# Kernel tuning notes

Measured on AMD Instinct MI355X. Metric: run time of the kernel, lower is better.

Reference implementation:

```python
import jax, jax.numpy as jnp
import numpy as np

EPS = 0.01  # diffusion sampling noise scale


def gru_last(x, Wx, Wh, bx, bh):
    """Run a single-layer GRU (torch gate conventions) over x: [B, L, C] -> final hidden [B, H]."""
    B, L, C = x.shape
    H = Wh.shape[0]
    xg = jnp.einsum('blc,cg->blg', x, Wx) + bx  # precomputed input gates [B, L, 3H]

    def step(h, xg_t):
        hg = h @ Wh + bh
        xr, xz, xn = jnp.split(xg_t, 3, axis=-1)
        hr, hz, hn = jnp.split(hg, 3, axis=-1)
        r = jax.nn.sigmoid(xr + hr)
        z = jax.nn.sigmoid(xz + hz)
        n = jnp.tanh(xn + r * hn)
        h_new = (1.0 - z) * n + z * h
        return h_new, None

    h0 = jnp.zeros((B, H), x.dtype)
    h, _ = jax.lax.scan(step, h0, jnp.swapaxes(xg, 0, 1))
    return h


def gru_aggr(x, Wx, Wh, bx, bh, Wo, bo):
    return gru_last(x, Wx, Wh, bx, bh) @ Wo + bo


def setup_inputs() -> dict:
    key = jax.random.key(0)
    N, C, DEG, H, C_OUT, T = 8000, 64, 16, 128, 64, 4
    ks = jax.random.split(key, 16)

    def lin(k, fan_in, shape):
        return jax.random.normal(k, shape, dtype=jnp.float32) / np.sqrt(fan_in)

    inp = {
        'node_attr': jax.random.normal(ks[0], (N, C), dtype=jnp.float32),
        'neighbors': jax.random.randint(ks[1], (N, DEG), 0, N, dtype=jnp.int32),
        'noise': jax.random.normal(ks[2], (T, N, DEG), dtype=jnp.float32),
        # diff_aggr GRU + output head (edge log-prob comes from channel 0)
        'dWx': lin(ks[3], C, (C, 3 * H)),
        'dWh': lin(ks[4], H, (H, 3 * H)),
        'dbx': jnp.zeros((3 * H,), jnp.float32),
        'dbh': jnp.zeros((3 * H,), jnp.float32),
        'dWo': lin(ks[5], H, (H, C_OUT)),
        'dbo': jnp.zeros((C_OUT,), jnp.float32),
        # walk_aggr GRU + output head (node embedding)
        'wWx': lin(ks[6], C, (C, 3 * H)),
        'wWh': lin(ks[7], H, (H, 3 * H)),
        'wbx': jnp.zeros((3 * H,), jnp.float32),
        'wbh': jnp.zeros((3 * H,), jnp.float32),
        'wWo': lin(ks[8], H, (H, C_OUT)),
        'wbo': jnp.zeros((C_OUT,), jnp.float32),
    }
    return inp


def reference(node_attr, neighbors, noise,
              dWx, dWh, dbx, dbh, dWo, dbo,
              wWx, wWh, wbx, wbh, wWo, wbo):
    N, C = node_attr.shape
    DEG = neighbors.shape[1]
    T = noise.shape[0]

    cur = jnp.arange(N)                      # current frontier of each walk
    walk_embeds = node_attr[:, None, :]      # [N, L, C], L grows each step
    logps = []
    for t in range(T):
        nbr = neighbors[cur]                 # [N, DEG] candidate next hops
        cand = node_attr[nbr]                # [N, DEG, C]
        L = walk_embeds.shape[1]
        prefix = jnp.broadcast_to(walk_embeds[:, None], (N, DEG, L, C))
        seq = jnp.concatenate([prefix, cand[:, :, None, :]], axis=2)  # [N, DEG, L+1, C]
        seq = seq.reshape(N * DEG, L + 1, C)
        logp = gru_aggr(seq, dWx, dWh, dbx, dbh, dWo, dbo)[:, 0].reshape(N, DEG)
        # per-source-node log-softmax normalizer (no_grad in original)
        norm = jax.lax.stop_gradient(jax.nn.logsumexp(logp, axis=1, keepdims=True))
        logp = logp - norm
        p = jnp.exp(logp)
        noisy = p + EPS * noise[t]
        sel = jnp.argmax(noisy, axis=1)      # scatter_max over each node's candidates
        logps.append(jnp.take_along_axis(logp, sel[:, None], axis=1)[:, 0])
        cur = jnp.take_along_axis(nbr, sel[:, None], axis=1)[:, 0]
        walk_embeds = jnp.concatenate([walk_embeds, node_attr[cur][:, None, :]], axis=1)

    walks_logp = jnp.stack(logps, axis=1)    # [N, T]
    v_out = gru_aggr(walk_embeds, wWx, wWh, wbx, wbh, wWo, wbo)  # [N, C_OUT]
    return v_out, walks_logp
```

## Files before the change

### kernel.cpp

```cpp
#include <hip/hip_runtime.h>
#include <math.h>

#define NN 8000
#define CD 64
#define DG 16
#define HD 128
#define G3 384
#define TT 4
#define MARGIN 4e-3f

#if __has_builtin(__builtin_amdgcn_rcpf)
#define RCP(x) __builtin_amdgcn_rcpf(x)
#else
#define RCP(x) (1.f/(x))
#endif

__device__ __forceinline__ float fsig (float x){ return RCP(1.f + __expf(-x)); }
__device__ __forceinline__ float ftanh(float x){ return 1.f - 2.f*RCP(1.f + __expf(2.f*x)); }

__device__ __forceinline__ double fexp64(double x){
    const double LOG2E  = 1.4426950408889634074;
    const double LN2_HI = 6.93147180369123816490e-01;
    const double LN2_LO = 1.90821492927058770002e-10;
    x = fmin(fmax(x, -700.0), 700.0);
    double fn = rint(x * LOG2E);
    double r  = fma(-fn, LN2_HI, x);
    r = fma(-fn, LN2_LO, r);
    double p = 1.6059043836821613e-10;
    p = fma(p, r, 2.0876756987868099e-09);
    p = fma(p, r, 2.5052108385441719e-08);
    p = fma(p, r, 2.7557319223985893e-07);
    p = fma(p, r, 2.7557319223985888e-06);
    p = fma(p, r, 2.4801587301587302e-05);
    p = fma(p, r, 1.9841269841269841e-04);
    p = fma(p, r, 1.3888888888888889e-03);
    p = fma(p, r, 8.3333333333333332e-03);
    p = fma(p, r, 4.1666666666666664e-02);
    p = fma(p, r, 1.6666666666666666e-01);
    p = fma(p, r, 0.5);
    p = fma(p, r, 1.0);
    p = fma(p, r, 1.0);
    long long bits = __double_as_longlong(p) + ((long long)(int)fn << 52);
    return __longlong_as_double(bits);
}
__device__ __forceinline__ double sig64f (double x){ return 1.0/(1.0 + fexp64(-x)); }
__device__ __forceinline__ double tanh64f(double x){ return 1.0 - 2.0/(fexp64(2.0*x) + 1.0); }

__global__ __launch_bounds__(384) void xg_kernel(const float* __restrict__ A,
    const float* __restrict__ W, const float* __restrict__ b,
    float* __restrict__ hiP, float* __restrict__ loP)
{
    __shared__ float a_s[8][64];
    const int g  = threadIdx.x;
    const int l  = g & 63, q = g >> 6;
    const int n0 = blockIdx.x * 8;
    for (int idx = threadIdx.x; idx < 8*64; idx += 384)
        a_s[idx>>6][idx&63] = A[(size_t)n0*64 + idx];
    __syncthreads();
    double acc[8];
    const double bg = (double)b[g];
#pragma unroll
    for (int j=0;j<8;j++) acc[j] = bg;
    for (int c=0;c<64;c++){
        const double w = (double)W[c*G3 + g];
#pragma unroll
        for (int j=0;j<8;j++) acc[j] += (double)a_s[j][c]*w;
    }
#pragma unroll
    for (int j=0;j<8;j++){
        const size_t base = (size_t)(n0+j)*64 + l;
        const float hi = (float)acc[j];
        hiP[base*8 + q] = hi;
        if (q < 2) hiP[base*8 + 6 + q] = 0.f;
        if (loP) loP[base*6 + q] = (float)(acc[j] - (double)hi);
    }
}

__global__ __launch_bounds__(256) void repack_kernel(const float* __restrict__ W,
                                                     float* __restrict__ P)
{
    const int idx = blockIdx.x*256 + threadIdx.x;
    const int k = idx >> 9, rem = idx & 511, l = rem >> 3, s = rem & 7;
    P[idx] = (s < 6) ? W[k*G3 + s*64 + l] : 0.f;
}

__global__ __launch_bounds__(256) void walk_kernel(
    const int*   __restrict__ nbrs,  const float* __restrict__ noise,
    const float* __restrict__ XGfP,  const float* __restrict__ dWhP,
    const float* __restrict__ dbh,   const float* __restrict__ dWo,
    const float* __restrict__ dbo,
    int* __restrict__ paths, int* __restrict__ fail_cnt, int* __restrict__ fail_list,
    float* __restrict__ out)
{
    __shared__ float hf_s[4][HD];
    __shared__ float part_s[4][4][6][64];

    const int wid  = threadIdx.x >> 6;
    const int lane = threadIdx.x & 63;
    const int node = blockIdx.x*4 + wid;

    float h0 = 0.f, h1 = 0.f;
    float dbhf[6], hgf[6];
#pragma unroll
    for (int m=0;m<6;m++){ dbhf[m] = dbh[lane+64*m]; hgf[m] = dbhf[m]; }
    const float wo0f0 = dWo[lane*CD];
    const float wo0f1 = dWo[(lane+64)*CD];
    const float dbo0f = dbo[0];

    int  cur = node;
    int  ch0=0, ch1=0, ch2=0, ch3=0;
    bool pushed = false;

    for (int t=0;t<TT;t++){
        if      (t==0) ch0 = cur;
        else if (t==1) ch1 = cur;
        else if (t==2) ch2 = cur;
        else           ch3 = cur;

        {
            const float4* xr = (const float4*)(XGfP + ((size_t)cur*64 + lane)*8);
            const float4 A = xr[0], B = xr[1];
            float r = fsig (A.x + hgf[0]);
            float z = fsig (A.z + hgf[2]);
            float n = ftanh(B.x + r*hgf[4]);
            h0 = (1.f-z)*n + z*h0;
            r = fsig (A.y + hgf[1]);
            z = fsig (A.w + hgf[3]);
            n = ftanh(B.y + r*hgf[5]);
            h1 = (1.f-z)*n + z*h1;
        }
        hf_s[wid][lane] = h0;  hf_s[wid][lane+64] = h1;
        __syncthreads();

        {
            float pacc[4][6];
#pragma unroll
            for (int j=0;j<4;j++)
#pragma unroll
                for (int m=0;m<6;m++) pacc[j][m] = 0.f;
            const float4* wr = (const float4*)(dWhP + (size_t)lane*8);
#pragma unroll 4
            for (int kk=0; kk<32; kk++){
                const int k = wid*32 + kk;
                const float4 W0 = wr[k*128], W1 = wr[k*128+1];
#pragma unroll
                for (int j=0;j<4;j++){
                    const float hk = hf_s[j][k];
                    pacc[j][0] += hk*W0.x; pacc[j][1] += hk*W0.y;
                    pacc[j][2] += hk*W0.z; pacc[j][3] += hk*W0.w;
                    pacc[j][4] += hk*W1.x; pacc[j][5] += hk*W1.y;
                }
            }
#pragma unroll
            for (int j=0;j<4;j++)
#pragma unroll
                for (int m=0;m<6;m++) part_s[wid][j][m][lane] = pacc[j][m];
        }
        __syncthreads();

#pragma unroll
        for (int m=0;m<6;m++)
            hgf[m] = dbhf[m] + part_s[0][wid][m][lane] + part_s[1][wid][m][lane]
                             + part_s[2][wid][m][lane] + part_s[3][wid][m][lane];

        int   nbrv = (lane < DG) ? nbrs[(size_t)cur*DG + lane] : 0;
        float nz   = (lane < DG) ? noise[((size_t)t*NN + node)*DG + lane] : 0.f;
        float lf = -3.0e38f;
#pragma unroll
        for (int g=0; g<4; g++){
            float4 CA[4], CB[4];
#pragma unroll
            for (int j=0;j<4;j++){
                const int nd = __shfl(nbrv, g*4+j);
                const float4* cr = (const float4*)(XGfP + ((size_t)nd*64 + lane)*8);
                CA[j] = cr[0];  CB[j] = cr[1];
            }
            float part[4];
#pragma unroll
            for (int j=0;j<4;j++){
                float r = fsig (CA[j].x + hgf[0]);
                float z = fsig (CA[j].z + hgf[2]);
                float n = ftanh(CB[j].x + r*hgf[4]);
                part[j]  = ((1.f-z)*n + z*h0) * wo0f0;
                r = fsig (CA[j].y + hgf[1]);
                z = fsig (CA[j].w + hgf[3]);
                n = ftanh(CB[j].y + r*hgf[5]);
                part[j] += ((1.f-z)*n + z*h1) * wo0f1;
            }
#pragma unroll
            for (int off=32; off>0; off>>=1){
#pragma unroll
                for (int j=0;j<4;j++) part[j] += __shfl_xor(part[j], off);
            }
#pragma unroll
            for (int j=0;j<4;j++) if (lane == g*4+j) lf = part[j] + dbo0f;
        }

        float v  = (lane < DG) ? lf : -3.0e38f;
        float mx = v;
#pragma unroll
        for (int off=32; off>0; off>>=1) mx = fmaxf(mx, __shfl_xor(mx, off));
        float e = (lane < DG) ? __expf(v - mx) : 0.f;
        float s = e;
#pragma unroll
        for (int off=32; off>0; off>>=1) s += __shfl_xor(s, off);
        const float normf = mx + __logf(s);

        float noisyf = (lane < DG) ? __expf(v - normf) + 0.01f*nz : -3.0e38f;
        int   idx = lane;
        float bv  = noisyf;
#pragma unroll
        for (int off=32; off>0; off>>=1){
            float ov = __shfl_xor(bv, off);
            int   oi = __shfl_xor(idx, off);
            if (ov > bv || (ov == bv && oi < idx)){ bv = ov; idx = oi; }
        }
        float sv = (lane == idx || lane >= DG) ? -3.0e38f : noisyf;
#pragma unroll
        for (int off=32; off>0; off>>=1) sv = fmaxf(sv, __shfl_xor(sv, off));

        const bool trip = (bv - sv) < MARGIN;
        if (trip && !pushed){
            if (lane == 0){
                const int slot = atomicAdd(fail_cnt, 1);
                if (slot < NN) fail_list[slot] = node | (t << 16);
            }
            pushed = true;
        }

        const float lpf = __shfl(v, idx) - normf;
        if (lane == 0) out[NN*CD + node*TT + t] = lpf;
        cur = __shfl(nbrv, idx);
    }

    if (lane == 0){
        int* p = paths + (size_t)node*8;
        p[0]=ch0; p[1]=ch1; p[2]=ch2; p[3]=ch3; p[4]=cur;
    }
}

__global__ __launch_bounds__(256) void fix_kernel(
    const int*   __restrict__ nbrs,  const float* __restrict__ noise,
    const float* __restrict__ XGfP,  const float* __restrict__ XGrP,
    const float* __restrict__ dWhP,  const float* __restrict__ dbh,
    const float* __restrict__ dWo,   const float* __restrict__ dbo,
    const int* __restrict__ fail_cnt, const int* __restrict__ fail_list,
    int* __restrict__ paths, float* __restrict__ out)
{
    __shared__ double h_s[4][HD];
    __shared__ double part_s[4][4][6][64];

    const int wid  = threadIdx.x >> 6;
    const int lane = threadIdx.x & 63;
    const int count = min(fail_cnt[0], NN);
    if (blockIdx.x*4 >= count) return;

    const int  ii     = blockIdx.x*4 + wid;
    const bool active = (ii < count);
    const int  entry  = active ? fail_list[ii] : fail_list[0];
    const int  node   = entry & 0xFFFF;
    const int  t0     = active ? (entry >> 16) : TT;
    const int* pw     = paths + (size_t)node*8;

    double db64[6];
#pragma unroll
    for (int m=0;m<6;m++) db64[m] = (double)dbh[lane+64*m];
    const double wo0d0 = (double)dWo[lane*CD];
    const double wo0d1 = (double)dWo[(lane+64)*CD];
    const double dbo0d = (double)dbo[0];

    double H0 = 0.0, H1 = 0.0;
    double g64[6];
#pragma unroll
    for (int m=0;m<6;m++) g64[m] = db64[m];
    int cur = node;
    int c0=0,c1=0,c2=0,c3=0;

    for (int t=0;t<TT;t++){
        if      (t==0) c0 = cur;
        else if (t==1) c1 = cur;
        else if (t==2) c2 = cur;
        else           c3 = cur;

        {
            const size_t base = (size_t)cur*64 + lane;
            const float* hi = XGfP + base*8;
            const float* lo = XGrP + base*6;
            double r = sig64f (((double)hi[0]+(double)lo[0]) + g64[0]);
            double z = sig64f (((double)hi[2]+(double)lo[2]) + g64[2]);
            double n = tanh64f(((double)hi[4]+(double)lo[4]) + r*g64[4]);
            H0 = (1.0-z)*n + z*H0;
            r = sig64f (((double)hi[1]+(double)lo[1]) + g64[1]);
            z = sig64f (((double)hi[3]+(double)lo[3]) + g64[3]);
            n = tanh64f(((double)hi[5]+(double)lo[5]) + r*g64[5]);
            H1 = (1.0-z)*n + z*H1;
        }
        h_s[wid][lane] = H0;  h_s[wid][lane+64] = H1;
        __syncthreads();

        {
            double pacc[4][6];
#pragma unroll
            for (int j=0;j<4;j++)
#pragma unroll
                for (int m=0;m<6;m++) pacc[j][m] = 0.0;
            const float4* wr = (const float4*)(dWhP + (size_t)lane*8);
#pragma unroll 4
            for (int kk=0; kk<32; kk++){
                const int k = wid*32 + kk;
                const float4 W0 = wr[k*128], W1 = wr[k*128+1];
#pragma unroll
                for (int j=0;j<4;j++){
                    const double hk = h_s[j][k];
                    pacc[j][0] += hk*(double)W0.x; pacc[j][1] += hk*(double)W0.y;
                    pacc[j][2] += hk*(double)W0.z; pacc[j][3] += hk*(double)W0.w;
                    pacc[j][4] += hk*(double)W1.x; pacc[j][5] += hk*(double)W1.y;
                }
            }
#pragma unroll
            for (int j=0;j<4;j++)
#pragma unroll
                for (int m=0;m<6;m++) part_s[wid][j][m][lane] = pacc[j][m];
        }
        __syncthreads();

#pragma unroll
        for (int m=0;m<6;m++)
            g64[m] = db64[m] + part_s[0][wid][m][lane] + part_s[1][wid][m][lane]
                             + part_s[2][wid][m][lane] + part_s[3][wid][m][lane];

        if (t < t0){
            cur = pw[t+1];
            continue;
        }

        int   nbrv = (lane < DG) ? nbrs[(size_t)cur*DG + lane] : 0;
        float nz   = (lane < DG) ? noise[((size_t)t*NN + node)*DG + lane] : 0.f;
        double lv = -1e300;
#pragma unroll
        for (int g=0; g<4; g++){
            float ch[4][6], cl[4][6];
#pragma unroll
            for (int j=0;j<4;j++){
                const int nd = __shfl(nbrv, g*4+j);
                const size_t base = (size_t)nd*64 + lane;
                const float* hi = XGfP + base*8;
                const float* lo = XGrP + base*6;
#pragma unroll
                for (int q=0;q<6;q++){ ch[j][q]=hi[q]; cl[j][q]=lo[q]; }
            }
#pragma unroll
            for (int j=0;j<4;j++){
                double r = sig64f (((double)ch[j][0]+(double)cl[j][0]) + g64[0]);
                double z = sig64f (((double)ch[j][2]+(double)cl[j][2]) + g64[2]);
                double n = tanh64f(((double)ch[j][4]+(double)cl[j][4]) + r*g64[4]);
                double part = ((1.0-z)*n + z*H0) * wo0d0;
                r = sig64f (((double)ch[j][1]+(double)cl[j][1]) + g64[1]);
                z = sig64f (((double)ch[j][3]+(double)cl[j][3]) + g64[3]);
                n = tanh64f(((double)ch[j][5]+(double)cl[j][5]) + r*g64[5]);
                part += ((1.0-z)*n + z*H1) * wo0d1;
#pragma unroll
                for (int off=32; off>0; off>>=1) part += __shfl_xor(part, off);
                if (lane == g*4+j) lv = part + dbo0d;
            }
        }

        double dv = (lane < DG) ? lv : -1e300;
        double dmx = dv;
#pragma unroll
        for (int off=32; off>0; off>>=1) dmx = fmax(dmx, __shfl_xor(dmx, off));
        double de = (lane < DG) ? fexp64(dv - dmx) : 0.0;
        double ds = de;
#pragma unroll
        for (int off=32; off>0; off>>=1) ds += __shfl_xor(ds, off);
        const double dnorm = dmx + log(ds);
        double dnoisy = (lane < DG) ? fexp64(dv - dnorm) + 0.01*(double)nz : -1e300;
        int di = lane;
#pragma unroll
        for (int off=32; off>0; off>>=1){
            double ov = __shfl_xor(dnoisy, off);
            int    oi = __shfl_xor(di, off);
            if (ov > dnoisy || (ov == dnoisy && oi < di)){ dnoisy = ov; di = oi; }
        }
        const double lpfix = __shfl(dv, di) - dnorm;
        if (active && lane == 0) out[NN*CD + node*TT + t] = (float)lpfix;
        cur = __shfl(nbrv, di);
    }

    if (active && lane == 0){
        int* p = paths + (size_t)node*8;
        p[0]=c0; p[1]=c1; p[2]=c2; p[3]=c3; p[4]=cur;
    }
}

__global__ __launch_bounds__(256) void wgru_kernel(
    const int*   __restrict__ paths, const float* __restrict__ XGwP,
    const float* __restrict__ wWhP,  const float* __restrict__ wbh,
    const float* __restrict__ wWo,   const float* __restrict__ wbo,
    float* __restrict__ out)
{
    __shared__ float hw_s[4][HD];
    __shared__ float part_s[4][4][6][64];
    const int wid  = threadIdx.x >> 6;
    const int lane = threadIdx.x & 63;
    const int node = blockIdx.x*4 + wid;

    float h0 = 0.f, h1 = 0.f;
    float wb[6], hg[6];
#pragma unroll
    for (int m=0;m<6;m++){ wb[m] = wbh[lane+64*m]; hg[m] = wb[m]; }
    const int* p = paths + (size_t)node*8;

#pragma unroll
    for (int s=0; s<=TT; s++){
        const int c = p[s];
        const float4* xr = (const float4*)(XGwP + ((size_t)c*64 + lane)*8);
        const float4 A = xr[0], B = xr[1];
        float r = fsig (A.x + hg[0]);
        float z = fsig (A.z + hg[2]);
        float n = ftanh(B.x + r*hg[4]);
        h0 = (1.f-z)*n + z*h0;
        r = fsig (A.y + hg[1]);
        z = fsig (A.w + hg[3]);
        n = ftanh(B.y + r*hg[5]);
        h1 = (1.f-z)*n + z*h1;
        if (s < TT){
            hw_s[wid][lane] = h0;  hw_s[wid][lane+64] = h1;
            __syncthreads();
            float pacc[4][6];
#pragma unroll
            for (int j=0;j<4;j++)
#pragma unroll
                for (int m=0;m<6;m++) pacc[j][m] = 0.f;
            const float4* wr = (const float4*)(wWhP + (size_t)lane*8);
#pragma unroll 4
            for (int kk=0; kk<32; kk++){
                const int k = wid*32 + kk;
                const float4 W0 = wr[k*128], W1 = wr[k*128+1];
#pragma unroll
                for (int j=0;j<4;j++){
                    const float hk = hw_s[j][k];
                    pacc[j][0] += hk*W0.x; pacc[j][1] += hk*W0.y;
                    pacc[j][2] += hk*W0.z; pacc[j][3] += hk*W0.w;
                    pacc[j][4] += hk*W1.x; pacc[j][5] += hk*W1.y;
                }
            }
#pragma unroll
            for (int j=0;j<4;j++)
#pragma unroll
                for (int m=0;m<6;m++) part_s[wid][j][m][lane] = pacc[j][m];
            __syncthreads();
#pragma unroll
            for (int m=0;m<6;m++)
                hg[m] = wb[m] + part_s[0][wid][m][lane] + part_s[1][wid][m][lane]
                              + part_s[2][wid][m][lane] + part_s[3][wid][m][lane];
        }
    }
    hw_s[wid][lane] = h0;  hw_s[wid][lane+64] = h1;
    __syncthreads();

    float acc = wbo[lane];
    const float* wcol = wWo + lane;
    for (int i=0;i<HD;i++) acc += hw_s[wid][i] * wcol[(size_t)i*CD];
    out[(size_t)node*CD + lane] = acc;
}

extern "C" void kernel_launch(void* const* d_in, const int* in_sizes, int n_in,
                              void* d_out, int out_size, void* d_ws, size_t ws_size,
                              hipStream_t stream)
{
    const float* attr  = (const float*)d_in[0];
    const int*   nbrs  = (const int*)  d_in[1];
    const float* noise = (const float*)d_in[2];
    const float* dWx = (const float*)d_in[3];
    const float* dWh = (const float*)d_in[4];
    const float* dbx = (const float*)d_in[5];
    const float* dbh = (const float*)d_in[6];
    const float* dWo = (const float*)d_in[7];
    const float* dbo = (const float*)d_in[8];
    const float* wWx = (const float*)d_in[9];
    const float* wWh = (const float*)d_in[10];
    const float* wbx = (const float*)d_in[11];
    const float* wbh = (const float*)d_in[12];
    const float* wWo = (const float*)d_in[13];
    const float* wbo = (const float*)d_in[14];
    float* out = (float*)d_out;

    char* ws = (char*)d_ws;
    float* XGfP      = (float*)(ws);
    float* XGrP      = (float*)(ws + 16384000);
    float* XGwP      = (float*)(ws + 28672000);
    float* dWhP      = (float*)(ws + 45056000);
    float* wWhP      = (float*)(ws + 45318144);
    int*   paths     = (int*)  (ws + 45580288);
    int*   fail_list = (int*)  (ws + 45836288);
    int*   fail_cnt  = (int*)  (ws + 45868288);

    hipMemsetAsync(fail_cnt, 0, sizeof(int), stream);

    xg_kernel<<<NN/8, G3, 0, stream>>>(attr, dWx, dbx, XGfP, XGrP);
    xg_kernel<<<NN/8, G3, 0, stream>>>(attr, wWx, wbx, XGwP, nullptr);
    repack_kernel<<<(HD*64*8)/256, 256, 0, stream>>>(dWh, dWhP);
    repack_kernel<<<(HD*64*8)/256, 256, 0, stream>>>(wWh, wWhP);

    walk_kernel<<<NN/4, 256, 0, stream>>>(nbrs, noise, XGfP, dWhP,
                                          dbh, dWo, dbo,
                                          paths, fail_cnt, fail_list, out);
    fix_kernel<<<2000, 256, 0, stream>>>(nbrs, noise, XGfP, XGrP,
                                         dWhP, dbh, dWo, dbo,
                                         fail_cnt, fail_list, paths, out);
    wgru_kernel<<<NN/4, 256, 0, stream>>>(paths, XGwP, wWhP, wbh, wWo, wbo, out);
}
```

Before: 529.1 us.

## Fuse fix-up and walk GRU into one tail kernel with per-node trip flags

Merges the fp64 fix-up pass and the walk-embedding GRU into a single launch. Non-tripped nodes run the walk GRU in their own blocks, while a fixed pool of blocks grid-strides over the failure list and runs the walk GRU right after recomputing each path. This removes one launch and serialization point, so fix-up work overlaps with the bulk walk GRU. The fp64 partial-sum reduction is also reshaped into two stages to cut shared memory, which adds extra syncs. In exchange, fix-up blocks now loop serially, so a long failure list could lengthen the tail.

```diff
diff --git a/kernel.cpp b/kernel.cpp
--- a/kernel.cpp
+++ b/kernel.cpp
@@ -8,6 +8,7 @@
 #define G3 384
 #define TT 4
 #define MARGIN 4e-3f
+#define FIXB 600
 
 #if __has_builtin(__builtin_amdgcn_rcpf)
 #define RCP(x) __builtin_amdgcn_rcpf(x)
@@ -90,7 +91,7 @@
     const float* __restrict__ dbh,   const float* __restrict__ dWo,
     const float* __restrict__ dbo,
     int* __restrict__ paths, int* __restrict__ fail_cnt, int* __restrict__ fail_list,
-    float* __restrict__ out)
+    int* __restrict__ trip_flag, float* __restrict__ out)
 {
     __shared__ float hf_s[4][HD];
     __shared__ float part_s[4][4][6][64];
@@ -236,184 +237,25 @@
     if (lane == 0){
         int* p = paths + (size_t)node*8;
         p[0]=ch0; p[1]=ch1; p[2]=ch2; p[3]=ch3; p[4]=cur;
-    }
-}
-
-__global__ __launch_bounds__(256) void fix_kernel(
-    const int*   __restrict__ nbrs,  const float* __restrict__ noise,
-    const float* __restrict__ XGfP,  const float* __restrict__ XGrP,
-    const float* __restrict__ dWhP,  const float* __restrict__ dbh,
-    const float* __restrict__ dWo,   const float* __restrict__ dbo,
-    const int* __restrict__ fail_cnt, const int* __restrict__ fail_list,
-    int* __restrict__ paths, float* __restrict__ out)
+        trip_flag[node] = pushed ? 1 : 0;
+    }
+}
+
+__device__ __forceinline__ void run_wgru4(
+    float* hwm, float* pbuf, const int* w5, const bool doWrite, const int node,
+    const float* __restrict__ XGwP, const float* __restrict__ wWhP,
+    const float* __restrict__ wbh,  const float* __restrict__ wWo,
+    const float* __restrict__ wbo,  float* __restrict__ out,
+    const int wid, const int lane)
 {
-    __shared__ double h_s[4][HD];
-    __shared__ double part_s[4][4][6][64];
-
-    const int wid  = threadIdx.x >> 6;
-    const int lane = threadIdx.x & 63;
-    const int count = min(fail_cnt[0], NN);
-    if (blockIdx.x*4 >= count) return;
-
-    const int  ii     = blockIdx.x*4 + wid;
-    const bool active = (ii < count);
-    const int  entry  = active ? fail_list[ii] : fail_list[0];
-    const int  node   = entry & 0xFFFF;
-    const int  t0     = active ? (entry >> 16) : TT;
-    const int* pw     = paths + (size_t)node*8;
-
-    double db64[6];
-#pragma unroll
-    for (int m=0;m<6;m++) db64[m] = (double)dbh[lane+64*m];
-    const double wo0d0 = (double)dWo[lane*CD];
-    const double wo0d1 = (double)dWo[(lane+64)*CD];
-    const double dbo0d = (double)dbo[0];
-
-    double H0 = 0.0, H1 = 0.0;
-    double g64[6];
-#pragma unroll
-    for (int m=0;m<6;m++) g64[m] = db64[m];
-    int cur = node;
-    int c0=0,c1=0,c2=0,c3=0;
-
-    for (int t=0;t<TT;t++){
-        if      (t==0) c0 = cur;
-        else if (t==1) c1 = cur;
-        else if (t==2) c2 = cur;
-        else           c3 = cur;
-
-        {
-            const size_t base = (size_t)cur*64 + lane;
-            const float* hi = XGfP + base*8;
-            const float* lo = XGrP + base*6;
-            double r = sig64f (((double)hi[0]+(double)lo[0]) + g64[0]);
-            double z = sig64f (((double)hi[2]+(double)lo[2]) + g64[2]);
-            double n = tanh64f(((double)hi[4]+(double)lo[4]) + r*g64[4]);
-            H0 = (1.0-z)*n + z*H0;
-            r = sig64f (((double)hi[1]+(double)lo[1]) + g64[1]);
-            z = sig64f (((double)hi[3]+(double)lo[3]) + g64[3]);
-            n = tanh64f(((double)hi[5]+(double)lo[5]) + r*g64[5]);
-            H1 = (1.0-z)*n + z*H1;
-        }
-        h_s[wid][lane] = H0;  h_s[wid][lane+64] = H1;
-        __syncthreads();
-
-        {
-            double pacc[4][6];
-#pragma unroll
-            for (int j=0;j<4;j++)
-#pragma unroll
-                for (int m=0;m<6;m++) pacc[j][m] = 0.0;
-            const float4* wr = (const float4*)(dWhP + (size_t)lane*8);
-#pragma unroll 4
-            for (int kk=0; kk<32; kk++){
-                const int k = wid*32 + kk;
-                const float4 W0 = wr[k*128], W1 = wr[k*128+1];
-#pragma unroll
-                for (int j=0;j<4;j++){
-                    const double hk = h_s[j][k];
-                    pacc[j][0] += hk*(double)W0.x; pacc[j][1] += hk*(double)W0.y;
-                    pacc[j][2] += hk*(double)W0.z; pacc[j][3] += hk*(double)W0.w;
-                    pacc[j][4] += hk*(double)W1.x; pacc[j][5] += hk*(double)W1.y;
-                }
-            }
-#pragma unroll
-            for (int j=0;j<4;j++)
-#pragma unroll
-                for (int m=0;m<6;m++) part_s[wid][j][m][lane] = pacc[j][m];
-        }
-        __syncthreads();
-
-#pragma unroll
-        for (int m=0;m<6;m++)
-            g64[m] = db64[m] + part_s[0][wid][m][lane] + part_s[1][wid][m][lane]
-                             + part_s[2][wid][m][lane] + part_s[3][wid][m][lane];
-
-        if (t < t0){
-            cur = pw[t+1];
-            continue;
-        }
-
-        int   nbrv = (lane < DG) ? nbrs[(size_t)cur*DG + lane] : 0;
-        float nz   = (lane < DG) ? noise[((size_t)t*NN + node)*DG + lane] : 0.f;
-        double lv = -1e300;
-#pragma unroll
-        for (int g=0; g<4; g++){
-            float ch[4][6], cl[4][6];
-#pragma unroll
-            for (int j=0;j<4;j++){
-                const int nd = __shfl(nbrv, g*4+j);
-                const size_t base = (size_t)nd*64 + lane;
-                const float* hi = XGfP + base*8;
-                const float* lo = XGrP + base*6;
-#pragma unroll
-                for (int q=0;q<6;q++){ ch[j][q]=hi[q]; cl[j][q]=lo[q]; }
-            }
-#pragma unroll
-            for (int j=0;j<4;j++){
-                double r = sig64f (((double)ch[j][0]+(double)cl[j][0]) + g64[0]);
-                double z = sig64f (((double)ch[j][2]+(double)cl[j][2]) + g64[2]);
-                double n = tanh64f(((double)ch[j][4]+(double)cl[j][4]) + r*g64[4]);
-                double part = ((1.0-z)*n + z*H0) * wo0d0;
-                r = sig64f (((double)ch[j][1]+(double)cl[j][1]) + g64[1]);
-                z = sig64f (((double)ch[j][3]+(double)cl[j][3]) + g64[3]);
-                n = tanh64f(((double)ch[j][5]+(double)cl[j][5]) + r*g64[5]);
-                part += ((1.0-z)*n + z*H1) * wo0d1;
-#pragma unroll
-                for (int off=32; off>0; off>>=1) part += __shfl_xor(part, off);
-                if (lane == g*4+j) lv = part + dbo0d;
-            }
-        }
-
-        double dv = (lane < DG) ? lv : -1e300;
-        double dmx = dv;
-#pragma unroll
-        for (int off=32; off>0; off>>=1) dmx = fmax(dmx, __shfl_xor(dmx, off));
-        double de = (lane < DG) ? fexp64(dv - dmx) : 0.0;
-        double ds = de;
-#pragma unroll
-        for (int off=32; off>0; off>>=1) ds += __shfl_xor(ds, off);
-        const double dnorm = dmx + log(ds);
-        double dnoisy = (lane < DG) ? fexp64(dv - dnorm) + 0.01*(double)nz : -1e300;
-        int di = lane;
-#pragma unroll
-        for (int off=32; off>0; off>>=1){
-            double ov = __shfl_xor(dnoisy, off);
-            int    oi = __shfl_xor(di, off);
-            if (ov > dnoisy || (ov == dnoisy && oi < di)){ dnoisy = ov; di = oi; }
-        }
-        const double lpfix = __shfl(dv, di) - dnorm;
-        if (active && lane == 0) out[NN*CD + node*TT + t] = (float)lpfix;
-        cur = __shfl(nbrv, di);
-    }
-
-    if (active && lane == 0){
-        int* p = paths + (size_t)node*8;
-        p[0]=c0; p[1]=c1; p[2]=c2; p[3]=c3; p[4]=cur;
-    }
-}
-
-__global__ __launch_bounds__(256) void wgru_kernel(
-    const int*   __restrict__ paths, const float* __restrict__ XGwP,
-    const float* __restrict__ wWhP,  const float* __restrict__ wbh,
-    const float* __restrict__ wWo,   const float* __restrict__ wbo,
-    float* __restrict__ out)
-{
-    __shared__ float hw_s[4][HD];
-    __shared__ float part_s[4][4][6][64];
-    const int wid  = threadIdx.x >> 6;
-    const int lane = threadIdx.x & 63;
-    const int node = blockIdx.x*4 + wid;
-
     float h0 = 0.f, h1 = 0.f;
     float wb[6], hg[6];
 #pragma unroll
     for (int m=0;m<6;m++){ wb[m] = wbh[lane+64*m]; hg[m] = wb[m]; }
-    const int* p = paths + (size_t)node*8;
 
 #pragma unroll
     for (int s=0; s<=TT; s++){
-        const int c = p[s];
+        const int c = w5[s];
         const float4* xr = (const float4*)(XGwP + ((size_t)c*64 + lane)*8);
         const float4 A = xr[0], B = xr[1];
         float r = fsig (A.x + hg[0]);
@@ -425,21 +267,21 @@
         n = ftanh(B.y + r*hg[5]);
         h1 = (1.f-z)*n + z*h1;
         if (s < TT){
-            hw_s[wid][lane] = h0;  hw_s[wid][lane+64] = h1;
+            hwm[wid*HD + lane] = h0;  hwm[wid*HD + lane + 64] = h1;
             __syncthreads();
             float pacc[4][6];
 #pragma unroll
             for (int j=0;j<4;j++)
 #pragma unroll
                 for (int m=0;m<6;m++) pacc[j][m] = 0.f;
-            const float4* wr = (const float4*)(wWhP + (size_t)lane*8);
+            const float4* wv = (const float4*)(wWhP + (size_t)lane*8);
 #pragma unroll 4
             for (int kk=0; kk<32; kk++){
                 const int k = wid*32 + kk;
-                const float4 W0 = wr[k*128], W1 = wr[k*128+1];
+                const float4 W0 = wv[k*128], W1 = wv[k*128+1];
 #pragma unroll
                 for (int j=0;j<4;j++){
-                    const float hk = hw_s[j][k];
+                    const float hk = hwm[j*HD + k];
                     pacc[j][0] += hk*W0.x; pacc[j][1] += hk*W0.y;
                     pacc[j][2] += hk*W0.z; pacc[j][3] += hk*W0.w;
                     pacc[j][4] += hk*W1.x; pacc[j][5] += hk*W1.y;
@@ -448,21 +290,212 @@
 #pragma unroll
             for (int j=0;j<4;j++)
 #pragma unroll
-                for (int m=0;m<6;m++) part_s[wid][j][m][lane] = pacc[j][m];
+                for (int m=0;m<6;m++) pbuf[((wid*4+j)*6+m)*64 + lane] = pacc[j][m];
             __syncthreads();
 #pragma unroll
             for (int m=0;m<6;m++)
-                hg[m] = wb[m] + part_s[0][wid][m][lane] + part_s[1][wid][m][lane]
-                              + part_s[2][wid][m][lane] + part_s[3][wid][m][lane];
-        }
-    }
-    hw_s[wid][lane] = h0;  hw_s[wid][lane+64] = h1;
-    __syncthreads();
-
+                hg[m] = wb[m] + pbuf[((0*4+wid)*6+m)*64 + lane]
+                              + pbuf[((1*4+wid)*6+m)*64 + lane]
+                              + pbuf[((2*4+wid)*6+m)*64 + lane]
+                              + pbuf[((3*4+wid)*6+m)*64 + lane];
+        }
+    }
+    hwm[wid*HD + lane] = h0;  hwm[wid*HD + lane + 64] = h1;
     float acc = wbo[lane];
     const float* wcol = wWo + lane;
-    for (int i=0;i<HD;i++) acc += hw_s[wid][i] * wcol[(size_t)i*CD];
-    out[(size_t)node*CD + lane] = acc;
+    for (int i=0;i<HD;i++) acc += hwm[wid*HD + i] * wcol[(size_t)i*CD];
+    if (doWrite) out[(size_t)node*CD + lane] = acc;
+}
+
+__global__ __launch_bounds__(256) void tail_kernel(
+    const int*   __restrict__ nbrs,  const float* __restrict__ noise,
+    const float* __restrict__ XGfP,  const float* __restrict__ XGrP,
+    const float* __restrict__ dWhP,  const float* __restrict__ dbh,
+    const float* __restrict__ dWo,   const float* __restrict__ dbo,
+    const float* __restrict__ XGwP,  const float* __restrict__ wWhP,
+    const float* __restrict__ wbh,   const float* __restrict__ wWo,
+    const float* __restrict__ wbo,
+    const int* __restrict__ fail_cnt, const int* __restrict__ fail_list,
+    const int* __restrict__ trip_flag,
+    int* __restrict__ paths, float* __restrict__ out)
+{
+    __shared__ double smem[3584];
+    const int wid  = threadIdx.x >> 6;
+    const int lane = threadIdx.x & 63;
+
+    if (blockIdx.x >= FIXB){
+        const int node = (blockIdx.x - FIXB)*4 + wid;
+        float* hwm  = (float*)smem;
+        float* pbuf = (float*)(smem + 256);
+        int w5[5];
+        const int* p = paths + (size_t)node*8;
+#pragma unroll
+        for (int s=0;s<5;s++) w5[s] = p[s];
+        const bool doW = (trip_flag[node] == 0);
+        run_wgru4(hwm, pbuf, w5, doW, node, XGwP, wWhP, wbh, wWo, wbo,
+                  out, wid, lane);
+        return;
+    }
+
+    double* h_s  = smem;
+    double* dbuf = smem + 512;
+    const int count = min(fail_cnt[0], NN);
+
+    double db64[6];
+#pragma unroll
+    for (int m=0;m<6;m++) db64[m] = (double)dbh[lane+64*m];
+    const double wo0d0 = (double)dWo[lane*CD];
+    const double wo0d1 = (double)dWo[(lane+64)*CD];
+    const double dbo0d = (double)dbo[0];
+
+    for (int base = blockIdx.x*4; base < count; base += FIXB*4){
+        const int  ii     = base + wid;
+        const bool active = (ii < count);
+        const int  entry  = active ? fail_list[ii] : 0;
+        const int  node   = entry & 0xFFFF;
+        const int  t0     = active ? (entry >> 16) : TT;
+        const int* pw     = paths + (size_t)node*8;
+
+        double H0 = 0.0, H1 = 0.0;
+        double g64[6];
+#pragma unroll
+        for (int m=0;m<6;m++) g64[m] = db64[m];
+        int cur = node;
+        int c0=0,c1=0,c2=0,c3=0;
+
+        for (int t=0;t<TT;t++){
+            if      (t==0) c0 = cur;
+            else if (t==1) c1 = cur;
+            else if (t==2) c2 = cur;
+            else           c3 = cur;
+
+            {
+                const size_t b = (size_t)cur*64 + lane;
+                const float* hi = XGfP + b*8;
+                const float* lo = XGrP + b*6;
+                double r = sig64f (((double)hi[0]+(double)lo[0]) + g64[0]);
+                double z = sig64f (((double)hi[2]+(double)lo[2]) + g64[2]);
+                double n = tanh64f(((double)hi[4]+(double)lo[4]) + r*g64[4]);
+                H0 = (1.0-z)*n + z*H0;
+                r = sig64f (((double)hi[1]+(double)lo[1]) + g64[1]);
+                z = sig64f (((double)hi[3]+(double)lo[3]) + g64[3]);
+                n = tanh64f(((double)hi[5]+(double)lo[5]) + r*g64[5]);
+                H1 = (1.0-z)*n + z*H1;
+            }
+            h_s[wid*HD + lane] = H0;  h_s[wid*HD + lane + 64] = H1;
+            __syncthreads();
+
+            double pacc[4][6];
+#pragma unroll
+            for (int j=0;j<4;j++)
+#pragma unroll
+                for (int m=0;m<6;m++) pacc[j][m] = 0.0;
+            {
+                const float4* wv = (const float4*)(dWhP + (size_t)lane*8);
+#pragma unroll 4
+                for (int kk=0; kk<32; kk++){
+                    const int k = wid*32 + kk;
+                    const float4 W0 = wv[k*128], W1 = wv[k*128+1];
+#pragma unroll
+                    for (int j=0;j<4;j++){
+                        const double hk = h_s[j*HD + k];
+                        pacc[j][0] += hk*(double)W0.x; pacc[j][1] += hk*(double)W0.y;
+                        pacc[j][2] += hk*(double)W0.z; pacc[j][3] += hk*(double)W0.w;
+                        pacc[j][4] += hk*(double)W1.x; pacc[j][5] += hk*(double)W1.y;
+                    }
+                }
+            }
+            if (wid >= 2){
+#pragma unroll
+                for (int j=0;j<4;j++)
+#pragma unroll
+                    for (int m=0;m<6;m++)
+                        dbuf[(((wid-2)*4+j)*6+m)*64 + lane] = pacc[j][m];
+            }
+            __syncthreads();
+            if (wid < 2){
+#pragma unroll
+                for (int j=0;j<4;j++)
+#pragma unroll
+                    for (int m=0;m<6;m++){
+                        pacc[j][m] += dbuf[((wid*4+j)*6+m)*64 + lane];
+                        dbuf[((wid*4+j)*6+m)*64 + lane] = pacc[j][m];
+                    }
+            }
+            __syncthreads();
+#pragma unroll
+            for (int m=0;m<6;m++)
+                g64[m] = db64[m] + dbuf[((0*4+wid)*6+m)*64 + lane]
+                                 + dbuf[((1*4+wid)*6+m)*64 + lane];
+
+            if (t < t0){
+                cur = pw[t+1];
+                continue;
+            }
+
+            int   nbrv = (lane < DG) ? nbrs[(size_t)cur*DG + lane] : 0;
+            float nz   = (lane < DG) ? noise[((size_t)t*NN + node)*DG + lane] : 0.f;
+            double lv = -1e300;
+#pragma unroll
+            for (int g=0; g<4; g++){
+                float ch[4][6], cl[4][6];
+#pragma unroll
+                for (int j=0;j<4;j++){
+                    const int nd = __shfl(nbrv, g*4+j);
+                    const size_t b = (size_t)nd*64 + lane;
+                    const float* hi = XGfP + b*8;
+                    const float* lo = XGrP + b*6;
+#pragma unroll
+                    for (int q=0;q<6;q++){ ch[j][q]=hi[q]; cl[j][q]=lo[q]; }
+                }
+#pragma unroll
+                for (int j=0;j<4;j++){
+                    double r = sig64f (((double)ch[j][0]+(double)cl[j][0]) + g64[0]);
+                    double z = sig64f (((double)ch[j][2]+(double)cl[j][2]) + g64[2]);
+                    double n = tanh64f(((double)ch[j][4]+(double)cl[j][4]) + r*g64[4]);
+                    double part = ((1.0-z)*n + z*H0) * wo0d0;
+                    r = sig64f (((double)ch[j][1]+(double)cl[j][1]) + g64[1]);
+                    z = sig64f (((double)ch[j][3]+(double)cl[j][3]) + g64[3]);
+                    n = tanh64f(((double)ch[j][5]+(double)cl[j][5]) + r*g64[5]);
+                    part += ((1.0-z)*n + z*H1) * wo0d1;
+#pragma unroll
+                    for (int off=32; off>0; off>>=1) part += __shfl_xor(part, off);
+                    if (lane == g*4+j) lv = part + dbo0d;
+                }
+            }
+
+            double dv = (lane < DG) ? lv : -1e300;
+            double dmx = dv;
+#pragma unroll
+            for (int off=32; off>0; off>>=1) dmx = fmax(dmx, __shfl_xor(dmx, off));
+            double de = (lane < DG) ? fexp64(dv - dmx) : 0.0;
+            double ds = de;
+#pragma unroll
+            for (int off=32; off>0; off>>=1) ds += __shfl_xor(ds, off);
+            const double dnorm = dmx + log(ds);
+            double dnoisy = (lane < DG) ? fexp64(dv - dnorm) + 0.01*(double)nz : -1e300;
+            int di = lane;
+#pragma unroll
+            for (int off=32; off>0; off>>=1){
+                double ov = __shfl_xor(dnoisy, off);
+                int    oi = __shfl_xor(di, off);
+                if (ov > dnoisy || (ov == dnoisy && oi < di)){ dnoisy = ov; di = oi; }
+            }
+            const double lpfix = __shfl(dv, di) - dnorm;
+            if (active && lane == 0) out[NN*CD + node*TT + t] = (float)lpfix;
+            cur = __shfl(nbrv, di);
+        }
+
+        const int w5[5] = {c0, c1, c2, c3, cur};
+        if (active && lane == 0){
+            int* p = paths + (size_t)node*8;
+            p[0]=c0; p[1]=c1; p[2]=c2; p[3]=c3; p[4]=cur;
+        }
+        __syncthreads();
+        run_wgru4((float*)smem, (float*)(smem + 256), w5, active, node,
+                  XGwP, wWhP, wbh, wWo, wbo, out, wid, lane);
+        __syncthreads();
+    }
 }
 
 extern "C" void kernel_launch(void* const* d_in, const int* in_sizes, int n_in,
@@ -494,7 +527,8 @@
     float* wWhP      = (float*)(ws + 45318144);
     int*   paths     = (int*)  (ws + 45580288);
     int*   fail_list = (int*)  (ws + 45836288);
-    int*   fail_cnt  = (int*)  (ws + 45868288);
+    int*   trip_flag = (int*)  (ws + 45868288);
+    int*   fail_cnt  = (int*)  (ws + 45900288);
 
     hipMemsetAsync(fail_cnt, 0, sizeof(int), stream);
 
@@ -505,9 +539,10 @@
 
     walk_kernel<<<NN/4, 256, 0, stream>>>(nbrs, noise, XGfP, dWhP,
                                           dbh, dWo, dbo,
-                                          paths, fail_cnt, fail_list, out);
-    fix_kernel<<<2000, 256, 0, stream>>>(nbrs, noise, XGfP, XGrP,
-                                         dWhP, dbh, dWo, dbo,
-                                         fail_cnt, fail_list, paths, out);
-    wgru_kernel<<<NN/4, 256, 0, stream>>>(paths, XGwP, wWhP, wbh, wWo, wbo, out);
-}
+                                          paths, fail_cnt, fail_list, trip_flag, out);
+    tail_kernel<<<FIXB + NN/4, 256, 0, stream>>>(nbrs, noise, XGfP, XGrP,
+                                                 dWhP, dbh, dWo, dbo,
+                                                 XGwP, wWhP, wbh, wWo, wbo,
+                                                 fail_cnt, fail_list, trip_flag,
+                                                 paths, out);
+}
```

After: 542.2 us. 1.02x slower.

## Record per-step trip mask and skip fp64 re-evaluation for non-tripped steps

Applied to the files above, without the earlier changes.

The fast float walk kernel now builds a bitmask of every step whose top-two margin is small and pushes the node once at the end, instead of pushing at the first trip. The fp64 fix kernel recomputes the candidate scoring only at flagged steps, or after its path has diverged from the stored one, and otherwise follows the stored path. This cuts the expensive double-precision neighbor evaluation for later non-tripped steps. The partial-sum reduction is also rewritten as a two-stage shared-memory tree with an extra barrier, which shrinks the shared-memory footprint to improve occupancy.

```diff
diff --git a/kernel.cpp b/kernel.cpp
--- a/kernel.cpp
+++ b/kernel.cpp
@@ -107,9 +107,9 @@
     const float wo0f1 = dWo[(lane+64)*CD];
     const float dbo0f = dbo[0];
 
-    int  cur = node;
-    int  ch0=0, ch1=0, ch2=0, ch3=0;
-    bool pushed = false;
+    int cur = node;
+    int ch0=0, ch1=0, ch2=0, ch3=0;
+    int tripmask = 0;
 
     for (int t=0;t<TT;t++){
         if      (t==0) ch0 = cur;
@@ -219,14 +219,7 @@
 #pragma unroll
         for (int off=32; off>0; off>>=1) sv = fmaxf(sv, __shfl_xor(sv, off));
 
-        const bool trip = (bv - sv) < MARGIN;
-        if (trip && !pushed){
-            if (lane == 0){
-                const int slot = atomicAdd(fail_cnt, 1);
-                if (slot < NN) fail_list[slot] = node | (t << 16);
-            }
-            pushed = true;
-        }
+        if ((bv - sv) < MARGIN) tripmask |= (1 << t);
 
         const float lpf = __shfl(v, idx) - normf;
         if (lane == 0) out[NN*CD + node*TT + t] = lpf;
@@ -236,6 +229,10 @@
     if (lane == 0){
         int* p = paths + (size_t)node*8;
         p[0]=ch0; p[1]=ch1; p[2]=ch2; p[3]=ch3; p[4]=cur;
+        if (tripmask){
+            const int slot = atomicAdd(fail_cnt, 1);
+            if (slot < NN) fail_list[slot] = node | (tripmask << 16);
+        }
     }
 }
 
@@ -247,8 +244,9 @@
     const int* __restrict__ fail_cnt, const int* __restrict__ fail_list,
     int* __restrict__ paths, float* __restrict__ out)
 {
-    __shared__ double h_s[4][HD];
-    __shared__ double part_s[4][4][6][64];
+    __shared__ double smem[3584];
+    double* h_s  = smem;
+    double* dbuf = smem + 512;
 
     const int wid  = threadIdx.x >> 6;
     const int lane = threadIdx.x & 63;
@@ -257,9 +255,9 @@
 
     const int  ii     = blockIdx.x*4 + wid;
     const bool active = (ii < count);
-    const int  entry  = active ? fail_list[ii] : fail_list[0];
+    const int  entry  = active ? fail_list[ii] : 0;
     const int  node   = entry & 0xFFFF;
-    const int  t0     = active ? (entry >> 16) : TT;
+    const int  mask   = active ? (entry >> 16) : 0;
     const int* pw     = paths + (size_t)node*8;
 
     double db64[6];
@@ -273,8 +271,9 @@
     double g64[6];
 #pragma unroll
     for (int m=0;m<6;m++) g64[m] = db64[m];
-    int cur = node;
-    int c0=0,c1=0,c2=0,c3=0;
+    int  cur = node;
+    int  c0=0,c1=0,c2=0,c3=0;
+    bool diverged = false;
 
     for (int t=0;t<TT;t++){
         if      (t==0) c0 = cur;
@@ -283,9 +282,9 @@
         else           c3 = cur;
 
         {
-            const size_t base = (size_t)cur*64 + lane;
-            const float* hi = XGfP + base*8;
-            const float* lo = XGrP + base*6;
+            const size_t b = (size_t)cur*64 + lane;
+            const float* hi = XGfP + b*8;
+            const float* lo = XGrP + b*6;
             double r = sig64f (((double)hi[0]+(double)lo[0]) + g64[0]);
             double z = sig64f (((double)hi[2]+(double)lo[2]) + g64[2]);
             double n = tanh64f(((double)hi[4]+(double)lo[4]) + r*g64[4]);
@@ -295,41 +294,53 @@
             n = tanh64f(((double)hi[5]+(double)lo[5]) + r*g64[5]);
             H1 = (1.0-z)*n + z*H1;
         }
-        h_s[wid][lane] = H0;  h_s[wid][lane+64] = H1;
+        h_s[wid*HD + lane] = H0;  h_s[wid*HD + lane + 64] = H1;
         __syncthreads();
 
+        double pacc[4][6];
+#pragma unroll
+        for (int j=0;j<4;j++)
+#pragma unroll
+            for (int m=0;m<6;m++) pacc[j][m] = 0.0;
         {
-            double pacc[4][6];
-#pragma unroll
-            for (int j=0;j<4;j++)
-#pragma unroll
-                for (int m=0;m<6;m++) pacc[j][m] = 0.0;
-            const float4* wr = (const float4*)(dWhP + (size_t)lane*8);
+            const float4* wv = (const float4*)(dWhP + (size_t)lane*8);
 #pragma unroll 4
             for (int kk=0; kk<32; kk++){
                 const int k = wid*32 + kk;
-                const float4 W0 = wr[k*128], W1 = wr[k*128+1];
+                const float4 W0 = wv[k*128], W1 = wv[k*128+1];
 #pragma unroll
                 for (int j=0;j<4;j++){
-                    const double hk = h_s[j][k];
+                    const double hk = h_s[j*HD + k];
                     pacc[j][0] += hk*(double)W0.x; pacc[j][1] += hk*(double)W0.y;
                     pacc[j][2] += hk*(double)W0.z; pacc[j][3] += hk*(double)W0.w;
                     pacc[j][4] += hk*(double)W1.x; pacc[j][5] += hk*(double)W1.y;
                 }
             }
+        }
+        if (wid >= 2){
 #pragma unroll
             for (int j=0;j<4;j++)
 #pragma unroll
-                for (int m=0;m<6;m++) part_s[wid][j][m][lane] = pacc[j][m];
+                for (int m=0;m<6;m++)
+                    dbuf[(((wid-2)*4+j)*6+m)*64 + lane] = pacc[j][m];
         }
         __syncthreads();
-
+        if (wid < 2){
+#pragma unroll
+            for (int j=0;j<4;j++)
+#pragma unroll
+                for (int m=0;m<6;m++){
+                    pacc[j][m] += dbuf[((wid*4+j)*6+m)*64 + lane];
+                    dbuf[((wid*4+j)*6+m)*64 + lane] = pacc[j][m];
+                }
+        }
+        __syncthreads();
 #pragma unroll
         for (int m=0;m<6;m++)
-            g64[m] = db64[m] + part_s[0][wid][m][lane] + part_s[1][wid][m][lane]
-                             + part_s[2][wid][m][lane] + part_s[3][wid][m][lane];
-
-        if (t < t0){
+            g64[m] = db64[m] + dbuf[((0*4+wid)*6+m)*64 + lane]
+                             + dbuf[((1*4+wid)*6+m)*64 + lane];
+
+        if (!diverged && !((mask >> t) & 1)){
             cur = pw[t+1];
             continue;
         }
@@ -343,9 +354,9 @@
 #pragma unroll
             for (int j=0;j<4;j++){
                 const int nd = __shfl(nbrv, g*4+j);
-                const size_t base = (size_t)nd*64 + lane;
-                const float* hi = XGfP + base*8;
-                const float* lo = XGrP + base*6;
+                const size_t b = (size_t)nd*64 + lane;
+                const float* hi = XGfP + b*8;
+                const float* lo = XGrP + b*6;
 #pragma unroll
                 for (int q=0;q<6;q++){ ch[j][q]=hi[q]; cl[j][q]=lo[q]; }
             }
@@ -384,7 +395,9 @@
         }
         const double lpfix = __shfl(dv, di) - dnorm;
         if (active && lane == 0) out[NN*CD + node*TT + t] = (float)lpfix;
-        cur = __shfl(nbrv, di);
+        const int newcur = __shfl(nbrv, di);
+        diverged = diverged || (newcur != pw[t+1]);
+        cur = newcur;
     }
 
     if (active && lane == 0){
```

After: 525.3 us. About the same (-0.7%).
